# Performance work log

Hardware: AMD Instinct MI355X
Metric: run time of the kernel (lower is better)

Reference implementation:

```python
import jax, jax.numpy as jnp
import numpy as np

T = 8          # temporal window (hardcoded '8' in the original)
N = 2048       # num_neurons
S = 8192       # num_synapses per neuron
MAXW = 8.0
UCAPTURE = 10.0 / 128.0
UMINUS = 10.0 / 128.0
USEARCH = 1.0 / 128.0
UBACKOFF = 96.0 / 128.0
UMIN = 4.0 / 128.0


def setup_inputs() -> dict:
    key = jax.random.key(0)
    k1, k2, k3 = jax.random.split(key, 3)
    all_input_spikes = jax.random.randint(k1, (T, N, S), 0, 2, dtype=jnp.int32)
    all_output_spikes = jax.random.randint(k2, (T, N), 0, 2, dtype=jnp.int32)
    W = jax.random.uniform(k3, (N, S), dtype=jnp.float32, minval=-0.5, maxval=8.5)
    return {"all_input_spikes": all_input_spikes,
            "all_output_spikes": all_output_spikes,
            "W": W}


def reference(all_input_spikes, all_output_spikes, W):
    # Clamp weights to [0, 8] (the two torch.where clamps).
    w = jnp.clip(W, 0.0, MAXW)  # [N, S]

    # Spike times encoded as 8 - (spike count over the temporal window).
    in_t = (8 - jnp.sum(all_input_spikes, axis=0)).astype(jnp.int32)        # [N, S]
    out_t = (8 - jnp.sum(all_output_spikes, axis=0)).astype(jnp.int32)[:, None]  # [N, 1]

    wn = w / MAXW
    p_plus = wn * (2.0 - wn)            # Bernoulli prob for fplus
    p_minus = (1.0 - wn) * (1.0 + wn)   # Bernoulli prob for fminus

    rk = jax.random.split(jax.random.key(42), 8)
    dt = w.dtype
    fplus = jax.random.bernoulli(rk[0], p_plus).astype(dt)
    fminus = jax.random.bernoulli(rk[1], p_minus).astype(dt)
    ucap = jax.random.bernoulli(rk[2], UCAPTURE, (N, S)).astype(dt)
    uminus = jax.random.bernoulli(rk[3], UMINUS, (N, S)).astype(dt)
    usearch = jax.random.bernoulli(rk[4], USEARCH, (N, S)).astype(dt)
    ubackoff = jax.random.bernoulli(rk[5], UBACKOFF, (N, S)).astype(dt)
    # umin is sampled independently in each of the four branches
    umin1 = jax.random.bernoulli(rk[6], UMIN, (N, S)).astype(dt)
    k7a, k7b, k7c = jax.random.split(rk[7], 3)
    umin2 = jax.random.bernoulli(k7a, UMIN, (N, S)).astype(dt)
    umin3 = jax.random.bernoulli(k7b, UMIN, (N, S)).astype(dt)
    umin4 = jax.random.bernoulli(k7c, UMIN, (N, S)).astype(dt)

    in_fired = in_t < 8
    out_fired = out_t < 8

    # Branch 1: capture (input at or before output)
    b1 = jnp.where(in_fired & out_fired & (in_t <= out_t),
                   w + ucap * jnp.maximum(fplus, umin1), w)
    # Branch 2: minus (input after output)
    b2 = jnp.where(in_fired & out_fired & (in_t > out_t),
                   b1 - uminus * jnp.maximum(fminus, umin2), b1)
    # Branch 3: search (input fired, output silent)
    b3 = jnp.where(in_fired & (out_t == 8),
                   b2 + usearch * jnp.maximum(fplus, umin3), b2)
    # Branch 4: backoff (input silent, output fired)
    b4 = jnp.where((in_t == 8) & out_fired,
                   b3 - ubackoff * jnp.maximum(fminus, umin4), b3)
    return b4
```

## Files before the change

### kernel.cpp

```cpp
#include <hip/hip_runtime.h>

#define TT 8
#define NN 2048
#define SS 8192
#define MM (NN * SS)

#define TH_CAP10  655360u
#define TH_SEARCH 65536u
#define TH_BACK   6291456u
#define TH_MIN    262144u

struct KeyPack { unsigned k[20]; };

__host__ __device__ __forceinline__ void tf2x32(unsigned k0, unsigned k1,
                                                unsigned x0, unsigned x1,
                                                unsigned& o0, unsigned& o1) {
  const unsigned ks2 = k0 ^ k1 ^ 0x1BD11BDAu;
  x0 += k0; x1 += k1;
#define TFR(r) { x0 += x1; x1 = (x1 << (r)) | (x1 >> (32 - (r))); x1 ^= x0; }
  TFR(13) TFR(15) TFR(26) TFR(6)
  x0 += k1;  x1 += ks2 + 1u;
  TFR(17) TFR(29) TFR(16) TFR(24)
  x0 += ks2; x1 += k0 + 2u;
  TFR(13) TFR(15) TFR(26) TFR(6)
  x0 += k0;  x1 += k1 + 3u;
  TFR(17) TFR(29) TFR(16) TFR(24)
  x0 += k1;  x1 += ks2 + 4u;
  TFR(13) TFR(15) TFR(26) TFR(6)
  x0 += ks2; x1 += k0 + 5u;
#undef TFR
  o0 = x0; o1 = x1;
}

__global__ __launch_bounds__(256) void ModSTDP_58823872086838_kernel(
    const int* __restrict__ inS,
    const int* __restrict__ outS,
    const float* __restrict__ W,
    float* __restrict__ out,
    KeyPack kp)
{
  const unsigned tid  = blockIdx.x * blockDim.x + threadIdx.x;
  const unsigned base = tid << 2;
  const unsigned n    = base >> 13;

  int osum = 0;
#pragma unroll
  for (int t = 0; t < TT; ++t) osum += outS[t * NN + n];
  const int  ot   = 8 - osum;
  const bool outF = ot < 8;

  const float4 w4 = *reinterpret_cast<const float4*>(W + base);

  int c0 = 0, c1 = 0, c2 = 0, c3 = 0;
#pragma unroll
  for (int t = 0; t < TT; ++t) {
    const int4 sp = *reinterpret_cast<const int4*>(inS + (size_t)t * MM + base);
    c0 += sp.x; c1 += sp.y; c2 += sp.z; c3 += sp.w;
  }
  const int   cnt[4] = {c0, c1, c2, c3};
  const float wv[4]  = {w4.x, w4.y, w4.z, w4.w};
  float res[4];

#pragma unroll
  for (int e = 0; e < 4; ++e) {
    const unsigned j = base + (unsigned)e;
    const float w = fminf(fmaxf(wv[e], 0.0f), 8.0f);
    const int  it  = 8 - cnt[e];
    const bool inF = it < 8;
    const bool b1 = inF && outF && (it <= ot);
    const bool b2 = inF && outF && (it > ot);
    const bool b3 = inF && !outF;
    const bool b4 = (!inF) && outF;
    const bool active = inF || outF;

    const float wn = w * 0.125f;
    const float pp = __fmul_rn(wn, __fsub_rn(2.0f, wn));
    const float pm = __fmul_rn(__fsub_rn(1.0f, wn), __fadd_rn(1.0f, wn));

    const bool useP = b1 || b3;
    const float    pA  = useP ? pp : pm;
    const unsigned ka0 = useP ? kp.k[0] : kp.k[2];
    const unsigned ka1 = useP ? kp.k[1] : kp.k[3];

    const unsigned kb0 = b1 ? kp.k[4]  : (b2 ? kp.k[6]  : (b3 ? kp.k[8]  : kp.k[10]));
    const unsigned kb1 = b1 ? kp.k[5]  : (b2 ? kp.k[7]  : (b3 ? kp.k[9]  : kp.k[11]));
    const unsigned thB = (b1 || b2) ? TH_CAP10 : (b3 ? TH_SEARCH : TH_BACK);
    const unsigned kc0 = b1 ? kp.k[12] : (b2 ? kp.k[14] : (b3 ? kp.k[16] : kp.k[18]));
    const unsigned kc1 = b1 ? kp.k[13] : (b2 ? kp.k[15] : (b3 ? kp.k[17] : kp.k[19]));

    unsigned a0, a1, bb0, bb1, cc0, cc1;
    tf2x32(ka0, ka1, 0u, j, a0, a1);
    const unsigned bitsA = a0 ^ a1;
    const float u = __uint_as_float((bitsA >> 9) | 0x3f800000u) - 1.0f;
    const bool fab = u < pA;

    tf2x32(kb0, kb1, 0u, j, bb0, bb1);
    const bool gate = (((bb0 ^ bb1) >> 9) < thB);

    tf2x32(kc0, kc1, 0u, j, cc0, cc1);
    const bool um = (((cc0 ^ cc1) >> 9) < TH_MIN);

    const bool doit = active && gate && (fab || um);
    const float sgn = (b2 || b4) ? -1.0f : 1.0f;
    res[e] = doit ? (w + sgn) : w;
  }

  *reinterpret_cast<float4*>(out + base) =
      make_float4(res[0], res[1], res[2], res[3]);
}

extern "C" void kernel_launch(void* const* d_in, const int* in_sizes, int n_in,
                              void* d_out, int out_size, void* d_ws, size_t ws_size,
                              hipStream_t stream) {
  const int*   inS  = (const int*)d_in[0];
  const int*   outS = (const int*)d_in[1];
  const float* W    = (const float*)d_in[2];
  float*       out  = (float*)d_out;

  unsigned rk[16];
  for (unsigned i = 0; i < 8; ++i) {
    unsigned o0, o1;
    tf2x32(0u, 42u, 0u, i, o0, o1);
    rk[2 * i] = o0; rk[2 * i + 1] = o1;
  }
  KeyPack kp;
  for (int i = 0; i < 14; ++i) kp.k[i] = rk[i];
  for (unsigned i = 0; i < 3; ++i) {
    unsigned o0, o1;
    tf2x32(rk[14], rk[15], 0u, i, o0, o1);
    kp.k[14 + 2 * i] = o0; kp.k[15 + 2 * i] = o1;
  }

  const int threads = MM / 4;
  dim3 block(256), grid(threads / 256);
  ModSTDP_58823872086838_kernel<<<grid, block, 0, stream>>>(inS, outS, W, out, kp);
}
```

Baseline: 134.8 us.

## Persistent grid-stride kernel with double-buffered loads and LDS key table

The main kernel becomes a persistent grid of 2048 blocks. Each thread walks tiles with a grid stride and prefetches the next tile's spikes and weights while it computes the current one, using nontemporal loads and stores. Per-neuron output spike counts move to a small pre-kernel. The branch-dependent key, threshold and sign selection is replaced with a four-row table held in LDS and indexed by a branch id. This trades an extra launch and higher register pressure from the double buffers for better overlap of memory and compute and fewer selects.

```diff
diff --git a/kernel.cpp b/kernel.cpp
--- a/kernel.cpp
+++ b/kernel.cpp
@@ -10,7 +10,15 @@
 #define TH_BACK   6291456u
 #define TH_MIN    262144u
 
-struct KeyPack { unsigned k[20]; };
+#define NBLOCKS   2048
+#define NTHREADS  (NBLOCKS * 256)
+#define ITERS     (MM / 4 / NTHREADS)
+
+typedef int   __attribute__((ext_vector_type(4))) intx4;
+typedef float __attribute__((ext_vector_type(4))) floatx4;
+typedef unsigned __attribute__((ext_vector_type(4))) uintx4;
+
+struct Tbl { unsigned v[32]; };
 
 __host__ __device__ __forceinline__ void tf2x32(unsigned k0, unsigned k1,
                                                 unsigned x0, unsigned x1,
@@ -32,81 +40,111 @@
   o0 = x0; o1 = x1;
 }
 
-__global__ __launch_bounds__(256) void ModSTDP_58823872086838_kernel(
-    const int* __restrict__ inS,
-    const int* __restrict__ outS,
-    const float* __restrict__ W,
-    float* __restrict__ out,
-    KeyPack kp)
-{
-  const unsigned tid  = blockIdx.x * blockDim.x + threadIdx.x;
-  const unsigned base = tid << 2;
-  const unsigned n    = base >> 13;
+__global__ __launch_bounds__(256) void ModSTDP_ocnt_kernel(
+    const int* __restrict__ outS, int* __restrict__ ocnt) {
+  const int n = blockIdx.x * blockDim.x + threadIdx.x;
+  int s = 0;
+#pragma unroll
+  for (int t = 0; t < TT; ++t) s += outS[t * NN + n];
+  ocnt[n] = s;
+}
 
-  int osum = 0;
+__device__ __forceinline__ void load_tile(const int* __restrict__ inS,
+                                          const int* __restrict__ ocnt,
+                                          const float* __restrict__ W,
+                                          unsigned base,
+                                          intx4 (&s)[TT], floatx4& w, int& o) {
 #pragma unroll
-  for (int t = 0; t < TT; ++t) osum += outS[t * NN + n];
-  const int  ot   = 8 - osum;
-  const bool outF = ot < 8;
+  for (int t = 0; t < TT; ++t)
+    s[t] = __builtin_nontemporal_load(
+        reinterpret_cast<const intx4*>(inS + (size_t)t * MM + base));
+  w = __builtin_nontemporal_load(reinterpret_cast<const floatx4*>(W + base));
+  o = ocnt[base >> 13];
+}
 
-  const float4 w4 = *reinterpret_cast<const float4*>(W + base);
-
-  int c0 = 0, c1 = 0, c2 = 0, c3 = 0;
+__device__ __forceinline__ void compute_tile(float* __restrict__ out,
+                                             const unsigned* __restrict__ tbl,
+                                             unsigned base,
+                                             const intx4 (&s)[TT],
+                                             const floatx4& w4, int o) {
+  int cnt[4] = {0, 0, 0, 0};
 #pragma unroll
   for (int t = 0; t < TT; ++t) {
-    const int4 sp = *reinterpret_cast<const int4*>(inS + (size_t)t * MM + base);
-    c0 += sp.x; c1 += sp.y; c2 += sp.z; c3 += sp.w;
+    cnt[0] += s[t].x; cnt[1] += s[t].y; cnt[2] += s[t].z; cnt[3] += s[t].w;
   }
-  const int   cnt[4] = {c0, c1, c2, c3};
-  const float wv[4]  = {w4.x, w4.y, w4.z, w4.w};
+  const float wv[4] = {w4.x, w4.y, w4.z, w4.w};
+  const bool outF = o > 0;
   float res[4];
-
 #pragma unroll
   for (int e = 0; e < 4; ++e) {
     const unsigned j = base + (unsigned)e;
     const float w = fminf(fmaxf(wv[e], 0.0f), 8.0f);
-    const int  it  = 8 - cnt[e];
-    const bool inF = it < 8;
-    const bool b1 = inF && outF && (it <= ot);
-    const bool b2 = inF && outF && (it > ot);
-    const bool b3 = inF && !outF;
-    const bool b4 = (!inF) && outF;
-    const bool active = inF || outF;
+    const int c = cnt[e];
+    const bool inF = c > 0;
+    const bool active = inF | outF;
+    const unsigned idx = inF ? (outF ? ((c >= o) ? 0u : 1u) : 2u) : 3u;
+
+    const uintx4 r0 = *reinterpret_cast<const uintx4*>(tbl + (idx << 3));
+    const uintx4 r1 = *reinterpret_cast<const uintx4*>(tbl + (idx << 3) + 4);
+    const unsigned ka0 = r0.x, ka1 = r0.y, kb0 = r0.z, kb1 = r0.w;
+    const unsigned kc0 = r1.x, kc1 = r1.y, thB = r1.z;
+    const float sgn = __uint_as_float(r1.w);
 
     const float wn = w * 0.125f;
     const float pp = __fmul_rn(wn, __fsub_rn(2.0f, wn));
     const float pm = __fmul_rn(__fsub_rn(1.0f, wn), __fadd_rn(1.0f, wn));
+    const float pA = (idx & 1u) ? pm : pp;
 
-    const bool useP = b1 || b3;
-    const float    pA  = useP ? pp : pm;
-    const unsigned ka0 = useP ? kp.k[0] : kp.k[2];
-    const unsigned ka1 = useP ? kp.k[1] : kp.k[3];
-
-    const unsigned kb0 = b1 ? kp.k[4]  : (b2 ? kp.k[6]  : (b3 ? kp.k[8]  : kp.k[10]));
-    const unsigned kb1 = b1 ? kp.k[5]  : (b2 ? kp.k[7]  : (b3 ? kp.k[9]  : kp.k[11]));
-    const unsigned thB = (b1 || b2) ? TH_CAP10 : (b3 ? TH_SEARCH : TH_BACK);
-    const unsigned kc0 = b1 ? kp.k[12] : (b2 ? kp.k[14] : (b3 ? kp.k[16] : kp.k[18]));
-    const unsigned kc1 = b1 ? kp.k[13] : (b2 ? kp.k[15] : (b3 ? kp.k[17] : kp.k[19]));
-
-    unsigned a0, a1, bb0, bb1, cc0, cc1;
+    unsigned a0, a1, b0, b1, c0, c1;
     tf2x32(ka0, ka1, 0u, j, a0, a1);
     const unsigned bitsA = a0 ^ a1;
     const float u = __uint_as_float((bitsA >> 9) | 0x3f800000u) - 1.0f;
     const bool fab = u < pA;
 
-    tf2x32(kb0, kb1, 0u, j, bb0, bb1);
-    const bool gate = (((bb0 ^ bb1) >> 9) < thB);
+    tf2x32(kb0, kb1, 0u, j, b0, b1);
+    const bool gate = (((b0 ^ b1) >> 9) < thB);
 
-    tf2x32(kc0, kc1, 0u, j, cc0, cc1);
-    const bool um = (((cc0 ^ cc1) >> 9) < TH_MIN);
+    tf2x32(kc0, kc1, 0u, j, c0, c1);
+    const bool um = (((c0 ^ c1) >> 9) < TH_MIN);
 
-    const bool doit = active && gate && (fab || um);
-    const float sgn = (b2 || b4) ? -1.0f : 1.0f;
-    res[e] = doit ? (w + sgn) : w;
+    const bool doit = active & gate & (fab | um);
+    res[e] = doit ? __fadd_rn(w, sgn) : w;
   }
+  floatx4 r;
+  r.x = res[0]; r.y = res[1]; r.z = res[2]; r.w = res[3];
+  __builtin_nontemporal_store(r, reinterpret_cast<floatx4*>(out + base));
+}
 
-  *reinterpret_cast<float4*>(out + base) =
-      make_float4(res[0], res[1], res[2], res[3]);
+__global__ __launch_bounds__(256) void ModSTDP_58823872086838_kernel(
+    const int* __restrict__ inS,
+    const int* __restrict__ ocnt,
+    const float* __restrict__ W,
+    float* __restrict__ out,
+    Tbl tb)
+{
+  __shared__ __align__(16) unsigned tbl[32];
+  if (threadIdx.x < 32) tbl[threadIdx.x] = tb.v[threadIdx.x];
+  __syncthreads();
+
+  const unsigned tid = blockIdx.x * blockDim.x + threadIdx.x;
+  const unsigned STRIDE = (unsigned)NTHREADS << 2;
+
+  intx4 sA[TT], sB[TT];
+  floatx4 wA, wB;
+  int oA, oB;
+
+  unsigned base = tid << 2;
+  load_tile(inS, ocnt, W, base, sA, wA, oA);
+
+#pragma unroll 1
+  for (int i = 0; i < ITERS; i += 2) {
+    load_tile(inS, ocnt, W, base + STRIDE, sB, wB, oB);
+    compute_tile(out, tbl, base, sA, wA, oA);
+    if (i + 2 < ITERS)
+      load_tile(inS, ocnt, W, base + 2 * STRIDE, sA, wA, oA);
+    compute_tile(out, tbl, base + STRIDE, sB, wB, oB);
+    base += 2 * STRIDE;
+  }
 }
 
 extern "C" void kernel_launch(void* const* d_in, const int* in_sizes, int n_in,
@@ -116,22 +154,36 @@
   const int*   outS = (const int*)d_in[1];
   const float* W    = (const float*)d_in[2];
   float*       out  = (float*)d_out;
+  int*         ocnt = (int*)d_ws;
 
-  unsigned rk[16];
-  for (unsigned i = 0; i < 8; ++i) {
-    unsigned o0, o1;
-    tf2x32(0u, 42u, 0u, i, o0, o1);
-    rk[2 * i] = o0; rk[2 * i + 1] = o1;
-  }
-  KeyPack kp;
-  for (int i = 0; i < 14; ++i) kp.k[i] = rk[i];
-  for (unsigned i = 0; i < 3; ++i) {
-    unsigned o0, o1;
-    tf2x32(rk[14], rk[15], 0u, i, o0, o1);
-    kp.k[14 + 2 * i] = o0; kp.k[15 + 2 * i] = o1;
+  unsigned kp[20];
+  {
+    unsigned rk[16];
+    for (unsigned i = 0; i < 8; ++i) {
+      unsigned o0, o1;
+      tf2x32(0u, 42u, 0u, i, o0, o1);
+      rk[2 * i] = o0; rk[2 * i + 1] = o1;
+    }
+    for (int i = 0; i < 14; ++i) kp[i] = rk[i];
+    for (unsigned i = 0; i < 3; ++i) {
+      unsigned o0, o1;
+      tf2x32(rk[14], rk[15], 0u, i, o0, o1);
+      kp[14 + 2 * i] = o0; kp[15 + 2 * i] = o1;
+    }
   }
 
-  const int threads = MM / 4;
-  dim3 block(256), grid(threads / 256);
-  ModSTDP_58823872086838_kernel<<<grid, block, 0, stream>>>(inS, outS, W, out, kp);
+  Tbl tb;
+  unsigned* v = tb.v;
+  v[0] = kp[0];  v[1] = kp[1];  v[2] = kp[4];   v[3] = kp[5];
+  v[4] = kp[12]; v[5] = kp[13]; v[6] = TH_CAP10; v[7] = 0x3f800000u;
+  v[8] = kp[2];  v[9] = kp[3];  v[10] = kp[6];  v[11] = kp[7];
+  v[12] = kp[14]; v[13] = kp[15]; v[14] = TH_CAP10; v[15] = 0xbf800000u;
+  v[16] = kp[0]; v[17] = kp[1]; v[18] = kp[8];  v[19] = kp[9];
+  v[20] = kp[16]; v[21] = kp[17]; v[22] = TH_SEARCH; v[23] = 0x3f800000u;
+  v[24] = kp[2]; v[25] = kp[3]; v[26] = kp[10]; v[27] = kp[11];
+  v[28] = kp[18]; v[29] = kp[19]; v[30] = TH_BACK; v[31] = 0xbf800000u;
+
+  ModSTDP_ocnt_kernel<<<dim3(NN / 256), dim3(256), 0, stream>>>(outS, ocnt);
+  ModSTDP_58823872086838_kernel<<<dim3(NBLOCKS), dim3(256), 0, stream>>>(
+      inS, ocnt, W, out, tb);
 }
```

After: 136.4 us. No clear change (+1.2%).
